# Optimization experiments

Measured on AMD Instinct MI355X. Metric: run time of the kernel, lower is better.

Reference implementation:

```python
import jax, jax.numpy as jnp
import numpy as np

H = 2048        # hidden_size
E = 8           # num_experts
TOPK = 2
I = 1408        # moe_intermediate_size
IS = 5632       # shared_expert_intermediate_size
NORM_TOPK = True


def setup_inputs() -> dict:
    key = jax.random.key(0)
    ks = jax.random.split(key, 9)
    s = lambda k, shape: jax.random.normal(k, shape, dtype=jnp.float32) * (1.0 / np.sqrt(shape[-2] if len(shape) > 1 else shape[-1]))
    return {
        "hidden_states": jax.random.normal(ks[0], (1, 512, H), dtype=jnp.float32),
        "gate_w": jax.random.normal(ks[1], (E, H), dtype=jnp.float32) * 0.02,   # router Linear(H->E), no bias
        "w_gate": s(ks[2], (E, H, I)),   # expert gate_proj
        "w_up": s(ks[3], (E, H, I)),     # expert up_proj
        "w_down": s(ks[4], (E, I, H)),   # expert down_proj
        "sh_gate_w": s(ks[5], (H, IS)),  # shared expert gate_proj
        "sh_up_w": s(ks[6], (H, IS)),    # shared expert up_proj
        "sh_down_w": s(ks[7], (IS, H)),  # shared expert down_proj
        "shexp_gate_w": jax.random.normal(ks[8], (H, 1), dtype=jnp.float32) * 0.02,  # shared_expert_gate Linear(H->1)
    }


def reference(hidden_states, gate_w, w_gate, w_up, w_down,
              sh_gate_w, sh_up_w, sh_down_w, shexp_gate_w):
    B, S, _ = hidden_states.shape
    x = hidden_states.reshape(-1, H)                      # [T, H]
    T = x.shape[0]

    # --- router: softmax over all experts, then top-k (moe_gating_topk_softmax) ---
    router_logits = x @ gate_w.T                          # [T, E]
    probs = jax.nn.softmax(router_logits, axis=-1)
    routing_weights, selected_experts = jax.lax.top_k(probs, TOPK)  # [T, K]
    if NORM_TOPK:
        routing_weights = routing_weights / jnp.sum(routing_weights, axis=-1, keepdims=True)

    # dense combine weights: combine[t, e] = routing weight if expert e selected for token t else 0
    combine = jnp.zeros((T, E), dtype=x.dtype)
    combine = combine.at[jnp.arange(T)[:, None], selected_experts].set(routing_weights)

    # --- experts: SwiGLU MLP per expert, vectorized over E ---
    g = jnp.einsum('th,ehi->tei', x, w_gate)              # [T, E, I]
    u = jnp.einsum('th,ehi->tei', x, w_up)                # [T, E, I]
    h = jax.nn.silu(g) * u                                # [T, E, I]
    expert_out = jnp.einsum('tei,eih,te->th', h, w_down, combine)  # weighted scatter-add

    # --- shared expert with sigmoid gate ---
    sh = jax.nn.silu(x @ sh_gate_w) * (x @ sh_up_w)       # [T, IS]
    shared_out = (sh @ sh_down_w) * jax.nn.sigmoid(x @ shexp_gate_w)  # [T, H]

    out = (expert_out + shared_out).reshape(B, S, H)
    return (out, router_logits)
```

## Files before the change

### kernel.cpp

```cpp
#include <hip/hip_runtime.h>
#include <hip/hip_bf16.h>

#define NT  512
#define NH  2048
#define NE  8
#define NI  1408
#define NIS 5632

typedef __bf16 bf16x8 __attribute__((ext_vector_type(8)));
typedef float  f32x4  __attribute__((ext_vector_type(4)));

#define GLDS(gp, lp) __builtin_amdgcn_global_load_lds( \
    (const __attribute__((address_space(1))) void*)(gp), \
    (__attribute__((address_space(3))) void*)(lp), 16, 0, 0)

static constexpr size_t WS_XBF  = 0;
static constexpr size_t WS_SEL  = WS_XBF + (size_t)NT*NH*2;
static constexpr size_t WS_WTS  = WS_SEL + 4096;
static constexpr size_t WS_CNT  = WS_WTS + 4096;
static constexpr size_t WS_OFFE = WS_CNT + 32;
static constexpr size_t WS_TOK  = WS_OFFE + 32;
static constexpr size_t WS_PWT  = WS_TOK + 4096;
static constexpr size_t WS_SLOT = WS_PWT + 4096;
static constexpr size_t WS_G    = WS_SLOT + 4096;
static constexpr size_t WS_U    = WS_G   + (size_t)1024*NI*2;
static constexpr size_t WS_HBF  = WS_U   + (size_t)1024*NI*2;
static constexpr size_t WS_PAIR = WS_HBF + (size_t)1024*NI*2;
static constexpr size_t WS_SHG  = WS_PAIR+ (size_t)1024*NH*2;
static constexpr size_t WS_SHU  = WS_SHG + (size_t)NT*NIS*2;
static constexpr size_t WS_SHBF = WS_SHU + (size_t)NT*NIS*2;
static constexpr size_t WS_SHP  = WS_SHBF+ (size_t)NT*NIS*2;

__global__ void router_kernel(const float* __restrict__ x, const float* __restrict__ gw,
                              float* __restrict__ out_logits,
                              int* __restrict__ sel, float* __restrict__ wts)
{
    int w    = threadIdx.x >> 6;
    int lane = threadIdx.x & 63;
    int t    = blockIdx.x * 4 + w;
    int e    = lane & 7, c = lane >> 3;
    const float* xr = x  + (size_t)t * NH + c * 256;
    const float* gr = gw + (size_t)e * NH + c * 256;
    float acc = 0.f;
    #pragma unroll 8
    for (int it = 0; it < 64; ++it) {
        float4 xv = *(const float4*)(xr + it*4);
        float4 gv = *(const float4*)(gr + it*4);
        acc += xv.x*gv.x + xv.y*gv.y + xv.z*gv.z + xv.w*gv.w;
    }
    acc += __shfl_xor(acc, 8);
    acc += __shfl_xor(acc, 16);
    acc += __shfl_xor(acc, 32);
    if (lane < 8) out_logits[(size_t)t * NE + e] = acc;

    float l[8];
    #pragma unroll
    for (int j = 0; j < 8; ++j) l[j] = __shfl(acc, j);
    if (lane == 0) {
        int i1 = 0;
        #pragma unroll
        for (int j = 1; j < 8; ++j) if (l[j] > l[i1]) i1 = j;
        int i2 = -1;
        #pragma unroll
        for (int j = 0; j < 8; ++j) {
            if (j == i1) continue;
            if (i2 < 0 || l[j] > l[i2]) i2 = j;
        }
        float d  = expf(l[i2] - l[i1]);
        float w1 = 1.f / (1.f + d);
        float w2 = 1.f - w1;
        sel[2*t]   = i1;  sel[2*t+1] = i2;
        wts[2*t]   = w1;  wts[2*t+1] = w2;
    }
}

__global__ void bucket_kernel(const int* __restrict__ sel, const float* __restrict__ wts,
                              int* __restrict__ cnt, int* __restrict__ offe,
                              int* __restrict__ tok, float* __restrict__ pwt,
                              int* __restrict__ slot)
{
    int tid  = threadIdx.x;
    int wid  = tid >> 6;
    int lane = tid & 63;
    __shared__ int scnt[8], soff[8];

    unsigned long long masks[16];
    int total = 0;
    #pragma unroll
    for (int c = 0; c < 16; ++c) {
        int idx = c * 64 + lane;
        int s = sel[idx];
        unsigned long long m = __ballot(s == wid);
        masks[c] = m;
        total += __popcll(m);
    }
    if (lane == 0) { scnt[wid] = total; cnt[wid] = total; }
    __syncthreads();
    if (tid == 0) {
        int s = 0;
        #pragma unroll
        for (int j = 0; j < 8; ++j) { soff[j] = s; offe[j] = s; s += scnt[j]; }
    }
    __syncthreads();
    int pfx = soff[wid];
    unsigned long long below = (lane == 63) ? ~0ull >> 1 : ((1ull << lane) - 1);
    #pragma unroll
    for (int c = 0; c < 16; ++c) {
        int idx = c * 64 + lane;
        unsigned long long m = masks[c];
        if ((m >> lane) & 1ull) {
            int rank = pfx + (int)__popcll(m & below);
            tok[rank]  = idx >> 1;
            pwt[rank]  = wts[idx];
            slot[idx]  = rank;
        }
        pfx += (int)__popcll(m);
    }
}

__global__ void cast_kernel(const float* __restrict__ src, __bf16* __restrict__ dst, long long n)
{
    long long i = ((long long)blockIdx.x * blockDim.x + threadIdx.x) * 4;
    if (i >= n) return;
    float4 v = *(const float4*)(src + i);
    __bf16 o[4] = { (__bf16)v.x, (__bf16)v.y, (__bf16)v.z, (__bf16)v.w };
    *(uint2*)(dst + i) = *(const uint2*)o;
}

__global__ void silu_fused_kernel(const __bf16* __restrict__ g1, const __bf16* __restrict__ u1,
                                  __bf16* __restrict__ h1, long long n1,
                                  const __bf16* __restrict__ g2, const __bf16* __restrict__ u2,
                                  __bf16* __restrict__ h2, long long n2)
{
    long long i = ((long long)blockIdx.x * blockDim.x + threadIdx.x) * 8;
    const __bf16 *g, *u; __bf16* h; long long idx;
    if (i < n1)           { g = g1; u = u1; h = h1; idx = i; }
    else if (i < n1 + n2) { g = g2; u = u2; h = h2; idx = i - n1; }
    else return;
    uint4 gv = *(const uint4*)(g + idx);
    uint4 uv = *(const uint4*)(u + idx);
    const __bf16* gp = (const __bf16*)&gv;
    const __bf16* up = (const __bf16*)&uv;
    __bf16 o[8];
    #pragma unroll
    for (int j = 0; j < 8; ++j) {
        float x = (float)gp[j];
        float y = x / (1.f + __expf(-x)) * (float)up[j];
        o[j] = (__bf16)y;
    }
    *(uint4*)(h + idx) = *(const uint4*)o;
}

template<int NK, bool GATHER>
__device__ __forceinline__ void gemm_core(char* __restrict__ smem,
    const __bf16* __restrict__ A, int lda,
    const float* __restrict__ B, int ldb,
    __bf16* __restrict__ C, int ldc,
    int rows, int base, const int* __restrict__ tok, int m0, int n0)
{
    const int tid  = threadIdx.x;
    const int lane = tid & 63;
    const int wid  = tid >> 6;
    const int wr   = wid >> 1, wc = wid & 1;

    const int rs0 = (wid*2 + 0)*16 + (lane >> 2);
    const int rs1 = (wid*2 + 1)*16 + (lane >> 2);
    const int cch = lane & 3;
    int ga0 = m0 + rs0, ga1 = m0 + rs1;
    int ar0, ar1;
    if (GATHER) {
        ar0 = tok[base + (ga0 < rows ? ga0 : 0)];
        ar1 = tok[base + (ga1 < rows ? ga1 : 0)];
    } else {
        ar0 = base + (ga0 < rows ? ga0 : 0);
        ar1 = base + (ga1 < rows ? ga1 : 0);
    }
    const __bf16* a0p = A + (size_t)ar0 * lda + (cch ^ (rs0 & 3)) * 8;
    const __bf16* a1p = A + (size_t)ar1 * lda + (cch ^ (rs1 & 3)) * 8;
    char* lA0 = smem + (wid*2 + 0) * 1024;
    char* lA1 = smem + (wid*2 + 1) * 1024;

    const float* bp = B + (size_t)(wid*8 + (lane >> 5)) * ldb + n0 + (lane & 31)*4;
    char* lF = smem + 16384 + wid * 4096;

#define STAGE(b, t)                                                  \
    {                                                                \
        GLDS(a0p + (size_t)(t)*32, lA0 + (b)*8192);                  \
        GLDS(a1p + (size_t)(t)*32, lA1 + (b)*8192);                  \
        const float* bt = bp + (size_t)(t)*32*ldb;                   \
        char* fb = lF + (b)*16384;                                   \
        GLDS(bt,             fb);                                    \
        GLDS(bt + 2*ldb,     fb + 1024);                             \
        GLDS(bt + 4*ldb,     fb + 2048);                             \
        GLDS(bt + 6*ldb,     fb + 3072);                             \
    }

    const int cn  = tid & 127;
    const int ckh = tid >> 7;
    const int csw = (cn >> 1) & 3;
    __bf16* bbuf = (__bf16*)(smem + 49152);
    char* bw0 = (char*)bbuf + cn*64 + (((ckh*2 + 0) ^ csw) * 16);
    char* bw1 = (char*)bbuf + cn*64 + (((ckh*2 + 1) ^ csw) * 16);

    const int fr = lane & 15, fq = lane >> 4;
    const int aoff = (wr*64 + fr)*64 + ((fq ^ (fr & 3)) * 16);
    const int boff = (wc*64 + fr)*64 + ((fq ^ ((fr >> 1) & 3)) * 16);

    f32x4 acc[4][4];
    #pragma unroll
    for (int i = 0; i < 4; ++i)
        #pragma unroll
        for (int j = 0; j < 4; ++j) acc[i][j] = f32x4{0.f,0.f,0.f,0.f};

    STAGE(0, 0);

    #pragma unroll 1
    for (int t = 0; t < NK; ++t) {
        if (t + 1 < NK) {
            STAGE((t + 1) & 1, t + 1);
            asm volatile("s_waitcnt vmcnt(6)" ::: "memory");
        } else {
            asm volatile("s_waitcnt vmcnt(0)" ::: "memory");
        }
        __builtin_amdgcn_s_barrier();

        {
            const float* fp = (const float*)(smem + 16384 + (t & 1)*16384) + ckh*16*128 + cn;
            __bf16 ob[16];
            #pragma unroll
            for (int j = 0; j < 16; ++j) ob[j] = (__bf16)fp[j * 128];
            *(uint4*)bw0 = ((const uint4*)ob)[0];
            *(uint4*)bw1 = ((const uint4*)ob)[1];
        }
        asm volatile("s_waitcnt lgkmcnt(0)" ::: "memory");
        __builtin_amdgcn_s_barrier();

        {
            const char* Ab = smem + (t & 1) * 8192;
            bf16x8 af[4], bfr[4];
            #pragma unroll
            for (int m = 0; m < 4; ++m) af[m]  = *(const bf16x8*)(Ab + aoff + m*1024);
            #pragma unroll
            for (int n = 0; n < 4; ++n) bfr[n] = *(const bf16x8*)((const char*)bbuf + boff + n*1024);
            __builtin_amdgcn_s_setprio(1);
            #pragma unroll
            for (int m = 0; m < 4; ++m)
                #pragma unroll
                for (int n = 0; n < 4; ++n)
                    acc[m][n] = __builtin_amdgcn_mfma_f32_16x16x32_bf16(af[m], bfr[n], acc[m][n], 0, 0, 0);
            __builtin_amdgcn_s_setprio(0);
        }
        asm volatile("s_waitcnt lgkmcnt(0)" ::: "memory");
        __builtin_amdgcn_s_barrier();
    }
#undef STAGE

    __bf16* ep = (__bf16*)(smem + wid * 9216);
    #pragma unroll
    for (int m = 0; m < 4; ++m)
        #pragma unroll
        for (int n = 0; n < 4; ++n)
            #pragma unroll
            for (int q = 0; q < 4; ++q)
                ep[(m*16 + fq*4 + q)*72 + n*16 + fr] = (__bf16)acc[m][n][q];

    const int grow = m0 + wr*64 + lane;
    if (grow < rows) {
        __bf16* cp = C + (size_t)(base + grow) * ldc + n0 + wc*64;
        const __bf16* rp = ep + lane * 72;
        #pragma unroll
        for (int j = 0; j < 8; ++j)
            *(uint4*)(cp + j*8) = *(const uint4*)(rp + j*8);
    }
}

__launch_bounds__(256, 2)
__global__ void gemm_p1(const __bf16* __restrict__ xbf,
                        const float* __restrict__ w_gate, const float* __restrict__ w_up,
                        const float* __restrict__ sh_gate, const float* __restrict__ sh_up,
                        __bf16* __restrict__ gbuf, __bf16* __restrict__ ubuf,
                        __bf16* __restrict__ shg, __bf16* __restrict__ shu,
                        const int* __restrict__ cnt, const int* __restrict__ offe,
                        const int* __restrict__ tok)
{
    __shared__ alignas(16) char smem[57344];
    int z = blockIdx.z;
    if (z < 16) {
        if (blockIdx.x >= NI/128) return;
        int e = z & 7;
        int rows = cnt[e], base = offe[e];
        int m0 = blockIdx.y * 128; if (m0 >= rows) return;
        const float* B = (z < 8 ? w_gate : w_up) + (size_t)e * NH * NI;
        __bf16* C = (z < 8 ? gbuf : ubuf);
        gemm_core<NH/32, true>(smem, xbf, NH, B, NI, C, NI,
                               rows, base, tok, m0, blockIdx.x * 128);
    } else {
        const float* B = (z == 16 ? sh_gate : sh_up);
        __bf16* C = (z == 16 ? shg : shu);
        gemm_core<NH/32, false>(smem, xbf, NH, B, NIS, C, NIS,
                                NT, 0, nullptr, blockIdx.y * 128, blockIdx.x * 128);
    }
}

__launch_bounds__(256, 2)
__global__ void gemm_p3(const __bf16* __restrict__ hbf, const __bf16* __restrict__ shbf,
                        const float* __restrict__ w_down, const float* __restrict__ sh_down,
                        __bf16* __restrict__ pair, __bf16* __restrict__ shp,
                        const int* __restrict__ cnt, const int* __restrict__ offe)
{
    __shared__ alignas(16) char smem[57344];
    int z = blockIdx.z;
    if (z < 8) {
        int rows = cnt[z], base = offe[z];
        int m0 = blockIdx.y * 128; if (m0 >= rows) return;
        gemm_core<NI/32, false>(smem, hbf, NI, w_down + (size_t)z * NI * NH, NH,
                                pair, NH, rows, base, nullptr, m0, blockIdx.x * 128);
    } else {
        int q = z - 8;
        gemm_core<NI/32, false>(smem, shbf + q * NI, NIS,
                                sh_down + (size_t)q * NI * NH, NH,
                                shp + (size_t)q * NT * NH, NH,
                                NT, 0, nullptr, blockIdx.y * 128, blockIdx.x * 128);
    }
}

__global__ void combine_kernel(const float* __restrict__ x, const float* __restrict__ shexp_w,
                               const __bf16* __restrict__ shp, const __bf16* __restrict__ pair_out,
                               const int* __restrict__ slot, const float* __restrict__ wts,
                               float* __restrict__ out)
{
    int t = blockIdx.x;
    int tid = threadIdx.x;
    const float* xr = x + (size_t)t * NH;

    float p = 0.f;
    #pragma unroll
    for (int j = 0; j < 8; ++j) {
        int k = tid * 8 + j;
        p += xr[k] * shexp_w[k];
    }
    __shared__ float red[256];
    red[tid] = p;
    __syncthreads();
    for (int s = 128; s > 0; s >>= 1) {
        if (tid < s) red[tid] += red[tid + s];
        __syncthreads();
    }
    float sig = 1.f / (1.f + expf(-red[0]));

    int   s0 = slot[2*t],   s1 = slot[2*t+1];
    float w0 = wts[2*t],    w1 = wts[2*t+1];
    const __bf16* pr0 = pair_out + (size_t)s0 * NH;
    const __bf16* pr1 = pair_out + (size_t)s1 * NH;
    const __bf16* sd  = shp + (size_t)t * NH;
    float* orow = out + (size_t)t * NH;
    const size_t PS = (size_t)NT * NH;
    for (int n = tid; n < NH; n += 256) {
        float sdv = (float)sd[n] + (float)sd[n + PS] + (float)sd[n + 2*PS] + (float)sd[n + 3*PS];
        orow[n] = sdv * sig + w0 * (float)pr0[n] + w1 * (float)pr1[n];
    }
}

extern "C" void kernel_launch(void* const* d_in, const int* in_sizes, int n_in,
                              void* d_out, int out_size, void* d_ws, size_t ws_size,
                              hipStream_t stream)
{
    const float* x       = (const float*)d_in[0];
    const float* gate_w  = (const float*)d_in[1];
    const float* w_gate  = (const float*)d_in[2];
    const float* w_up    = (const float*)d_in[3];
    const float* w_down  = (const float*)d_in[4];
    const float* sh_gate = (const float*)d_in[5];
    const float* sh_up   = (const float*)d_in[6];
    const float* sh_down = (const float*)d_in[7];
    const float* shexp_g = (const float*)d_in[8];

    float* out        = (float*)d_out;
    float* out_logits = out + (size_t)NT * NH;

    char* ws = (char*)d_ws;
    __bf16* xbf  = (__bf16*)(ws + WS_XBF);
    int*    sel  = (int*)  (ws + WS_SEL);
    float*  wts  = (float*)(ws + WS_WTS);
    int*    cnt  = (int*)  (ws + WS_CNT);
    int*    offe = (int*)  (ws + WS_OFFE);
    int*    tok  = (int*)  (ws + WS_TOK);
    float*  pwt  = (float*)(ws + WS_PWT);
    int*    slot = (int*)  (ws + WS_SLOT);
    __bf16* gbuf = (__bf16*)(ws + WS_G);
    __bf16* ubuf = (__bf16*)(ws + WS_U);
    __bf16* hbf  = (__bf16*)(ws + WS_HBF);
    __bf16* pair = (__bf16*)(ws + WS_PAIR);
    __bf16* shg  = (__bf16*)(ws + WS_SHG);
    __bf16* shu  = (__bf16*)(ws + WS_SHU);
    __bf16* shbf = (__bf16*)(ws + WS_SHBF);
    __bf16* shp  = (__bf16*)(ws + WS_SHP);
    (void)pwt; (void)in_sizes; (void)n_in; (void)out_size; (void)ws_size;

    router_kernel<<<dim3(128), dim3(256), 0, stream>>>(x, gate_w, out_logits, sel, wts);
    bucket_kernel<<<dim3(1), dim3(512), 0, stream>>>(sel, wts, cnt, offe, tok, pwt, slot);
    cast_kernel<<<dim3(1024), dim3(256), 0, stream>>>(x, xbf, (long long)NT * NH);

    gemm_p1<<<dim3(44, 4, 18), dim3(256), 0, stream>>>(
        xbf, w_gate, w_up, sh_gate, sh_up, gbuf, ubuf, shg, shu, cnt, offe, tok);

    silu_fused_kernel<<<dim3(2112), dim3(256), 0, stream>>>(
        gbuf, ubuf, hbf, (long long)1024 * NI,
        shg, shu, shbf, (long long)NT * NIS);

    gemm_p3<<<dim3(16, 4, 12), dim3(256), 0, stream>>>(
        hbf, shbf, w_down, sh_down, pair, shp, cnt, offe);

    combine_kernel<<<dim3(NT), dim3(256), 0, stream>>>(
        x, shexp_g, shp, pair, slot, wts, out);
}
```

Baseline: 224.2 us.

## Load fp32 B tiles into registers, triple-buffer A, and raise occupancy

The fp32 weight tiles no longer pass through an LDS staging area. Each thread loads them directly into registers two k-steps ahead, converts them to bf16, and writes them into two alternating LDS buffers. The A tile moves to a three-slot rotating LDS ring, and the MFMA work of one step overlaps the global loads and conversion for later steps. This cuts LDS use from 56KB to 40KB, which lets launch bounds rise to 4 blocks per CU, at the cost of more registers held by 32 prefetch floats per thread. The B leading dimension also becomes a template constant.

```diff
diff --git a/kernel.cpp b/kernel.cpp
--- a/kernel.cpp
+++ b/kernel.cpp
@@ -151,10 +151,10 @@
     *(uint4*)(h + idx) = *(const uint4*)o;
 }
 
-template<int NK, bool GATHER>
+template<int NK, int LDB, bool GATHER>
 __device__ __forceinline__ void gemm_core(char* __restrict__ smem,
     const __bf16* __restrict__ A, int lda,
-    const float* __restrict__ B, int ldb,
+    const float* __restrict__ B,
     __bf16* __restrict__ C, int ldc,
     int rows, int base, const int* __restrict__ tok, int m0, int n0)
 {
@@ -177,30 +177,37 @@
     }
     const __bf16* a0p = A + (size_t)ar0 * lda + (cch ^ (rs0 & 3)) * 8;
     const __bf16* a1p = A + (size_t)ar1 * lda + (cch ^ (rs1 & 3)) * 8;
-    char* lA0 = smem + (wid*2 + 0) * 1024;
-    char* lA1 = smem + (wid*2 + 1) * 1024;
-
-    const float* bp = B + (size_t)(wid*8 + (lane >> 5)) * ldb + n0 + (lane & 31)*4;
-    char* lF = smem + 16384 + wid * 4096;
-
-#define STAGE(b, t)                                                  \
+
+#define AGLDS(slot, t)                                               \
     {                                                                \
-        GLDS(a0p + (size_t)(t)*32, lA0 + (b)*8192);                  \
-        GLDS(a1p + (size_t)(t)*32, lA1 + (b)*8192);                  \
-        const float* bt = bp + (size_t)(t)*32*ldb;                   \
-        char* fb = lF + (b)*16384;                                   \
-        GLDS(bt,             fb);                                    \
-        GLDS(bt + 2*ldb,     fb + 1024);                             \
-        GLDS(bt + 4*ldb,     fb + 2048);                             \
-        GLDS(bt + 6*ldb,     fb + 3072);                             \
+        char* d0 = smem + (slot)*8192 + (wid*2 + 0)*1024;            \
+        char* d1 = smem + (slot)*8192 + (wid*2 + 1)*1024;            \
+        GLDS(a0p + (size_t)(t)*32, d0);                              \
+        GLDS(a1p + (size_t)(t)*32, d1);                              \
     }
 
     const int cn  = tid & 127;
     const int ckh = tid >> 7;
     const int csw = (cn >> 1) & 3;
-    __bf16* bbuf = (__bf16*)(smem + 49152);
-    char* bw0 = (char*)bbuf + cn*64 + (((ckh*2 + 0) ^ csw) * 16);
-    char* bw1 = (char*)bbuf + cn*64 + (((ckh*2 + 1) ^ csw) * 16);
+    const float* bp = B + (size_t)(ckh * 16) * LDB + n0 + cn;
+    char* bbuf0 = smem + 24576;
+    char* bbuf1 = smem + 32768;
+
+#define BLOAD(R, t)                                                  \
+    {                                                                \
+        const float* bq = bp + (size_t)(t) * 32 * LDB;               \
+        _Pragma("unroll")                                            \
+        for (int j = 0; j < 16; ++j) R[j] = bq[(size_t)j * LDB];     \
+    }
+
+#define CONVERT(R, bbase)                                            \
+    {                                                                \
+        __bf16 ob[16];                                               \
+        _Pragma("unroll")                                            \
+        for (int j = 0; j < 16; ++j) ob[j] = (__bf16)R[j];           \
+        *(uint4*)((bbase) + cn*64 + (((ckh*2 + 0) ^ csw) * 16)) = ((const uint4*)ob)[0]; \
+        *(uint4*)((bbase) + cn*64 + (((ckh*2 + 1) ^ csw) * 16)) = ((const uint4*)ob)[1]; \
+    }
 
     const int fr = lane & 15, fq = lane >> 4;
     const int aoff = (wr*64 + fr)*64 + ((fq ^ (fr & 3)) * 16);
@@ -212,48 +219,63 @@
         #pragma unroll
         for (int j = 0; j < 4; ++j) acc[i][j] = f32x4{0.f,0.f,0.f,0.f};
 
-    STAGE(0, 0);
-
+#define MFMAS(slot, bbase)                                           \
+    {                                                                \
+        const char* Ab = smem + (slot)*8192;                         \
+        bf16x8 af[4], bfr[4];                                        \
+        _Pragma("unroll")                                            \
+        for (int m = 0; m < 4; ++m) af[m]  = *(const bf16x8*)(Ab + aoff + m*1024); \
+        _Pragma("unroll")                                            \
+        for (int n = 0; n < 4; ++n) bfr[n] = *(const bf16x8*)((bbase) + boff + n*1024); \
+        __builtin_amdgcn_s_setprio(1);                               \
+        _Pragma("unroll")                                            \
+        for (int m = 0; m < 4; ++m)                                  \
+            _Pragma("unroll")                                        \
+            for (int n = 0; n < 4; ++n)                              \
+                acc[m][n] = __builtin_amdgcn_mfma_f32_16x16x32_bf16(af[m], bfr[n], acc[m][n], 0, 0, 0); \
+        __builtin_amdgcn_s_setprio(0);                               \
+    }
+
+    float b0[16], b1[16];
+
+    BLOAD(b0, 0); AGLDS(0, 0);
+    BLOAD(b1, 1); AGLDS(1, 1);
+    asm volatile("s_waitcnt vmcnt(18)" ::: "memory");
+    CONVERT(b0, bbuf0);
+    asm volatile("s_waitcnt lgkmcnt(0)" ::: "memory");
+    __builtin_amdgcn_s_barrier();
+
+    int sA = 0, sB = 1, sC = 2;
     #pragma unroll 1
-    for (int t = 0; t < NK; ++t) {
-        if (t + 1 < NK) {
-            STAGE((t + 1) & 1, t + 1);
-            asm volatile("s_waitcnt vmcnt(6)" ::: "memory");
-        } else {
-            asm volatile("s_waitcnt vmcnt(0)" ::: "memory");
-        }
+    for (int t = 0; t < NK; t += 2) {
+        if (t + 2 < NK) { BLOAD(b0, t + 2); AGLDS(sC, t + 2); }
+        __builtin_amdgcn_sched_barrier(0);
+        MFMAS(sA, bbuf0);
+        __builtin_amdgcn_sched_barrier(0);
+        if (t + 2 < NK) asm volatile("s_waitcnt vmcnt(18)" ::: "memory");
+        else            asm volatile("s_waitcnt vmcnt(0)"  ::: "memory");
+        CONVERT(b1, bbuf1);
+        asm volatile("s_waitcnt lgkmcnt(0)" ::: "memory");
         __builtin_amdgcn_s_barrier();
 
-        {
-            const float* fp = (const float*)(smem + 16384 + (t & 1)*16384) + ckh*16*128 + cn;
-            __bf16 ob[16];
-            #pragma unroll
-            for (int j = 0; j < 16; ++j) ob[j] = (__bf16)fp[j * 128];
-            *(uint4*)bw0 = ((const uint4*)ob)[0];
-            *(uint4*)bw1 = ((const uint4*)ob)[1];
+        if (t + 3 < NK) { BLOAD(b1, t + 3); AGLDS(sA, t + 3); }
+        __builtin_amdgcn_sched_barrier(0);
+        MFMAS(sB, bbuf1);
+        __builtin_amdgcn_sched_barrier(0);
+        if (t + 2 < NK) {
+            if (t + 3 < NK) asm volatile("s_waitcnt vmcnt(18)" ::: "memory");
+            else            asm volatile("s_waitcnt vmcnt(0)"  ::: "memory");
+            CONVERT(b0, bbuf0);
         }
         asm volatile("s_waitcnt lgkmcnt(0)" ::: "memory");
         __builtin_amdgcn_s_barrier();
 
-        {
-            const char* Ab = smem + (t & 1) * 8192;
-            bf16x8 af[4], bfr[4];
-            #pragma unroll
-            for (int m = 0; m < 4; ++m) af[m]  = *(const bf16x8*)(Ab + aoff + m*1024);
-            #pragma unroll
-            for (int n = 0; n < 4; ++n) bfr[n] = *(const bf16x8*)((const char*)bbuf + boff + n*1024);
-            __builtin_amdgcn_s_setprio(1);
-            #pragma unroll
-            for (int m = 0; m < 4; ++m)
-                #pragma unroll
-                for (int n = 0; n < 4; ++n)
-                    acc[m][n] = __builtin_amdgcn_mfma_f32_16x16x32_bf16(af[m], bfr[n], acc[m][n], 0, 0, 0);
-            __builtin_amdgcn_s_setprio(0);
-        }
-        asm volatile("s_waitcnt lgkmcnt(0)" ::: "memory");
-        __builtin_amdgcn_s_barrier();
-    }
-#undef STAGE
+        int tmp = sA; sA = sC; sC = sB; sB = tmp;
+    }
+#undef AGLDS
+#undef BLOAD
+#undef CONVERT
+#undef MFMAS
 
     __bf16* ep = (__bf16*)(smem + wid * 9216);
     #pragma unroll
@@ -274,7 +296,7 @@
     }
 }
 
-__launch_bounds__(256, 2)
+__launch_bounds__(256, 4)
 __global__ void gemm_p1(const __bf16* __restrict__ xbf,
                         const float* __restrict__ w_gate, const float* __restrict__ w_up,
                         const float* __restrict__ sh_gate, const float* __restrict__ sh_up,
@@ -283,7 +305,7 @@
                         const int* __restrict__ cnt, const int* __restrict__ offe,
                         const int* __restrict__ tok)
 {
-    __shared__ alignas(16) char smem[57344];
+    __shared__ alignas(16) char smem[40960];
     int z = blockIdx.z;
     if (z < 16) {
         if (blockIdx.x >= NI/128) return;
@@ -292,35 +314,35 @@
         int m0 = blockIdx.y * 128; if (m0 >= rows) return;
         const float* B = (z < 8 ? w_gate : w_up) + (size_t)e * NH * NI;
         __bf16* C = (z < 8 ? gbuf : ubuf);
-        gemm_core<NH/32, true>(smem, xbf, NH, B, NI, C, NI,
-                               rows, base, tok, m0, blockIdx.x * 128);
+        gemm_core<NH/32, NI, true>(smem, xbf, NH, B, C, NI,
+                                   rows, base, tok, m0, blockIdx.x * 128);
     } else {
         const float* B = (z == 16 ? sh_gate : sh_up);
         __bf16* C = (z == 16 ? shg : shu);
-        gemm_core<NH/32, false>(smem, xbf, NH, B, NIS, C, NIS,
-                                NT, 0, nullptr, blockIdx.y * 128, blockIdx.x * 128);
-    }
-}
-
-__launch_bounds__(256, 2)
+        gemm_core<NH/32, NIS, false>(smem, xbf, NH, B, C, NIS,
+                                     NT, 0, nullptr, blockIdx.y * 128, blockIdx.x * 128);
+    }
+}
+
+__launch_bounds__(256, 4)
 __global__ void gemm_p3(const __bf16* __restrict__ hbf, const __bf16* __restrict__ shbf,
                         const float* __restrict__ w_down, const float* __restrict__ sh_down,
                         __bf16* __restrict__ pair, __bf16* __restrict__ shp,
                         const int* __restrict__ cnt, const int* __restrict__ offe)
 {
-    __shared__ alignas(16) char smem[57344];
+    __shared__ alignas(16) char smem[40960];
     int z = blockIdx.z;
     if (z < 8) {
         int rows = cnt[z], base = offe[z];
         int m0 = blockIdx.y * 128; if (m0 >= rows) return;
-        gemm_core<NI/32, false>(smem, hbf, NI, w_down + (size_t)z * NI * NH, NH,
-                                pair, NH, rows, base, nullptr, m0, blockIdx.x * 128);
+        gemm_core<NI/32, NH, false>(smem, hbf, NI, w_down + (size_t)z * NI * NH,
+                                    pair, NH, rows, base, nullptr, m0, blockIdx.x * 128);
     } else {
         int q = z - 8;
-        gemm_core<NI/32, false>(smem, shbf + q * NI, NIS,
-                                sh_down + (size_t)q * NI * NH, NH,
-                                shp + (size_t)q * NT * NH, NH,
-                                NT, 0, nullptr, blockIdx.y * 128, blockIdx.x * 128);
+        gemm_core<NI/32, NH, false>(smem, shbf + q * NI, NIS,
+                                    sh_down + (size_t)q * NI * NH,
+                                    shp + (size_t)q * NT * NH, NH,
+                                    NT, 0, nullptr, blockIdx.y * 128, blockIdx.x * 128);
     }
 }
 
```

Measured after the change: 741.8 us. 231% more time.
